# Kernel optimization log

Measured on AMD Instinct MI355X. Metric: run time of the kernel, lower is better.

The kernel has to match this reference:

```python
import jax, jax.numpy as jnp
import numpy as np

B, N, X_DIM, Y_DIM = 256, 128, 8, 8
Z_DIM, R_DIM, HID = 64, 128, 256
STEPS = 50
SIGMA_SQ = 0.5 ** 2
EPSILON = 1.0


def setup_inputs() -> dict:
    key = jax.random.key(0)
    ks = jax.random.split(key, 20)
    s = lambda fan_in: 1.0 / np.sqrt(fan_in)
    inp = {
        'x_ctx': jax.random.normal(ks[0], (B, N, X_DIM), jnp.float32),
        'y_ctx': jax.random.normal(ks[1], (B, N, Y_DIM), jnp.float32),
        'mask': jnp.ones((B, N, 1), jnp.float32),
        'z0': jax.random.normal(ks[2], (B, Z_DIM), jnp.float32),
        'noise': jax.random.normal(ks[3], (STEPS, B, Z_DIM), jnp.float32),
        # encoder: pointwise MLP on [x,y] then masked mean pool, project to r_dim
        'We1': jax.random.normal(ks[4], (X_DIM + Y_DIM, HID), jnp.float32) * s(X_DIM + Y_DIM),
        'be1': jnp.zeros((HID,), jnp.float32),
        'We2': jax.random.normal(ks[5], (HID, R_DIM), jnp.float32) * s(HID),
        'be2': jnp.zeros((R_DIM,), jnp.float32),
        # decoder: MLP([x, z]) -> y per context point
        'Wd1': jax.random.normal(ks[6], (X_DIM + Z_DIM, HID), jnp.float32) * s(X_DIM + Z_DIM),
        'bd1': jnp.zeros((HID,), jnp.float32),
        'Wd2': jax.random.normal(ks[7], (HID, Y_DIM), jnp.float32) * s(HID),
        'bd2': jnp.zeros((Y_DIM,), jnp.float32),
        # drift net: MLP([z, r, t]) -> z_dim
        'Wb1': jax.random.normal(ks[8], (Z_DIM + R_DIM + 1, HID), jnp.float32) * s(Z_DIM + R_DIM + 1),
        'bb1': jnp.zeros((HID,), jnp.float32),
        'Wb2': jax.random.normal(ks[9], (HID, Z_DIM), jnp.float32) * s(HID),
        'bb2': jnp.zeros((Z_DIM,), jnp.float32),
    }
    return inp


def _encode(x, y, mask, We1, be1, We2, be2):
    phi = jax.nn.gelu(jnp.concatenate([x, y], axis=-1) @ We1 + be1)  # [B,N,H]
    pooled = (phi * mask).sum(axis=1) / jnp.maximum(mask.sum(axis=1), 1.0)  # [B,H]
    return pooled @ We2 + be2  # [B,R]


def _decode(z, x, Wd1, bd1, Wd2, bd2):
    zb = jnp.broadcast_to(z[:, None, :], (z.shape[0], x.shape[1], z.shape[1]))
    h = jax.nn.gelu(jnp.concatenate([x, zb], axis=-1) @ Wd1 + bd1)  # [B,N,H]
    return h @ Wd2 + bd2  # [B,N,Y]


def _drift(z, r, t_col, Wb1, bb1, Wb2, bb2):
    h = jax.nn.gelu(jnp.concatenate([z, r, t_col], axis=-1) @ Wb1 + bb1)
    return h @ Wb2 + bb2  # [B,Z]


def reference(x_ctx, y_ctx, mask, z0, noise,
              We1, be1, We2, be2, Wd1, bd1, Wd2, bd2, Wb1, bb1, Wb2, bb2):
    dt = 1.0 / STEPS
    r = _encode(x_ctx, y_ctx, mask, We1, be1, We2, be2)  # [B,R]

    def energy_sum(z, t):
        u0 = 0.5 * jnp.sum(z ** 2, axis=1)  # [B]
        mu_y = _decode(z, x_ctx, Wd1, bd1, Wd2, bd2)
        sse = jnp.sum(((y_ctx - mu_y) ** 2) * mask, axis=(1, 2))  # [B]
        u1 = 0.5 * sse / SIGMA_SQ + u0
        return jnp.sum((1.0 - t) * u0 + t * u1)

    grad_energy = jax.grad(energy_sum, argnums=0)
    t_steps = (jnp.arange(STEPS, dtype=jnp.float32) * dt)
    noise_scale = jnp.sqrt(jnp.float32(2.0 * EPSILON * dt))

    def step(z, xs):
        t_curr, eps_noise = xs
        grad_u = jnp.clip(grad_energy(z, t_curr), -100.0, 100.0)
        t_col = jnp.full((z.shape[0], 1), t_curr, dtype=z.dtype)
        b = _drift(z, r, t_col, Wb1, bb1, Wb2, bb2)
        dz = (-EPSILON * grad_u + b) * dt + noise_scale * eps_noise
        return z + dz, None

    z_final, _ = jax.lax.scan(step, z0, (t_steps, noise))
    return z_final
```

## Files before the change

### kernel.cpp

```cpp
#include <hip/hip_runtime.h>
#include <math.h>

#define BB    256
#define NN_   128
#define ZD    64
#define RD    128
#define HID   256
#define NSTEPS 50
#define NT    16
#define NTILES 8
#define TPB   1024
#define PADD  258

__device__ __forceinline__ double fast_exp_d(double x) {
    const double L2E   = 1.44269504088896340736;
    const double LN2HI = 6.93147180369123816490e-01;
    const double LN2LO = 1.90821492927058770002e-10;
    const double MAGIC = 6755399441055744.0;
    double vn = fma(x, L2E, MAGIC);
    int ni = __double2loint(vn);
    double n = vn - MAGIC;
    double r = fma(n, -LN2HI, x);
    r = fma(n, -LN2LO, r);
    double p = 2.50521083854417187751e-08;
    p = fma(p, r, 2.75573192239858906526e-07);
    p = fma(p, r, 2.75573192239858906526e-06);
    p = fma(p, r, 2.48015873015873015873e-05);
    p = fma(p, r, 1.98412698412698412698e-04);
    p = fma(p, r, 1.38888888888888888889e-03);
    p = fma(p, r, 8.33333333333333333333e-03);
    p = fma(p, r, 4.16666666666666666667e-02);
    p = fma(p, r, 1.66666666666666666667e-01);
    p = fma(p, r, 0.5);
    p = fma(p, r, 1.0);
    p = fma(p, r, 1.0);
    return p * __hiloint2double((1023 + ni) << 20, 0);
}

__device__ __forceinline__ double sigmoid_d(double w) {
    double wc = fmin(fmax(w, -60.0), 60.0);
    double e = fast_exp_d(-wc);
    double d = 1.0 + e;
    float r0 = __builtin_amdgcn_rcpf((float)d);
    double y = (double)r0;
    y = fma(y, fma(-d, y, 1.0), y);
    y = fma(y, fma(-d, y, 1.0), y);
    return y;
}

__device__ __forceinline__ double gelu_d(double x) {
    const double c2 = 1.59576912160573071176;
    double w = c2 * x * fma(0.044715, x * x, 1.0);
    return x * sigmoid_d(w);
}

__device__ __forceinline__ void gelu_both_d(double x, double& h, double& gp) {
    const double c  = 0.79788456080286535588;
    const double a  = 0.044715;
    double x2 = x * x;
    double w  = (2.0 * c) * x * fma(a, x2, 1.0);
    double hp = sigmoid_d(w);
    h = x * hp;
    double s = hp * (1.0 - hp);
    gp = fma(x * s, (2.0 * c) * fma(3.0 * a, x2, 1.0), hp);
}

struct Smem {
    double h_t[NT][PADD];
    float  wd2t_f[8][PADD];
    double z_ds[ZD];
    double hb_ds[HID];
    double scratch4[4][HID];
    double pmgz[1024];
    double res_r[NT][8];
    double bp_d[16][ZD];
    double bd2_d[8];
    double bb2_d[ZD];
    double hbt_s[HID];
    double wbt_s[HID];
    float  bd1_s[HID];
    float  x_s[NN_][8];
    float  y_s[NN_][8];
    float  m_s[NN_];
    __align__(16) float4 wd1z4[HID][16];
};

__global__ void __launch_bounds__(TPB)
nets_sampler_kernel(
    const float* __restrict__ x_ctx, const float* __restrict__ y_ctx,
    const float* __restrict__ mask,  const float* __restrict__ z0,
    const float* __restrict__ noise,
    const float* __restrict__ We1, const float* __restrict__ be1,
    const float* __restrict__ We2, const float* __restrict__ be2,
    const float* __restrict__ Wd1, const float* __restrict__ bd1,
    const float* __restrict__ Wd2, const float* __restrict__ bd2,
    const float* __restrict__ Wb1, const float* __restrict__ bb1,
    const float* __restrict__ Wb2, const float* __restrict__ bb2,
    float* __restrict__ out)
{
    extern __shared__ char smem_raw[];
    Smem& sm = *reinterpret_cast<Smem*>(smem_raw);

    const int b   = blockIdx.x;
    const int tid = threadIdx.x;
    const int j   = tid & 255;
    const int q2  = tid >> 8;
    const int du_k = tid & 63, du_c = tid >> 6;
    double* r_d = &sm.res_r[0][0];

    if (tid < 256) {
        reinterpret_cast<float4*>(&sm.x_s[0][0])[tid] =
            reinterpret_cast<const float4*>(x_ctx + (size_t)b * NN_ * 8)[tid];
        reinterpret_cast<float4*>(&sm.y_s[0][0])[tid] =
            reinterpret_cast<const float4*>(y_ctx + (size_t)b * NN_ * 8)[tid];
        sm.bd1_s[j] = bd1[j];
        float4 a0 = reinterpret_cast<const float4*>(Wd2 + (size_t)j * 8)[0];
        float4 a1 = reinterpret_cast<const float4*>(Wd2 + (size_t)j * 8)[1];
        sm.wd2t_f[0][j] = a0.x; sm.wd2t_f[1][j] = a0.y;
        sm.wd2t_f[2][j] = a0.z; sm.wd2t_f[3][j] = a0.w;
        sm.wd2t_f[4][j] = a1.x; sm.wd2t_f[5][j] = a1.y;
        sm.wd2t_f[6][j] = a1.z; sm.wd2t_f[7][j] = a1.w;
    }
    if (tid < NN_) sm.m_s[tid] = mask[(size_t)b * NN_ + tid];
    if (tid < ZD) {
        sm.z_ds[tid]  = (double)z0[(size_t)b * ZD + tid];
        sm.bb2_d[tid] = (double)bb2[tid];
    }
    if (tid < 8) sm.bd2_d[tid] = (double)bd2[tid];

#pragma unroll
    for (int kk = 0; kk < 16; kk++) {
        const int k = q2 * 16 + kk;
        const float v = Wd1[(8 + k) * HID + j];
        reinterpret_cast<float*>(&sm.wd1z4[j][0])[4 * ((k >> 2) ^ (j & 15)) + (k & 3)] = v;
    }

    float wd1x[8];
#pragma unroll
    for (int k = 0; k < 8; k++) wd1x[k] = Wd1[k * HID + j];

    __syncthreads();

    if (tid < 256) {
        float we1r[16];
#pragma unroll
        for (int k = 0; k < 16; k++) we1r[k] = We1[k * HID + j];
        double be1_d = (double)be1[j];
        double msum = 0.0;
        for (int n = 0; n < NN_; n++) msum += (double)sm.m_s[n];
        msum = fmax(msum, 1.0);
        double pacc = 0.0;
        for (int n = 0; n < NN_; n++) {
            double pre = be1_d;
#pragma unroll
            for (int k = 0; k < 8; k++) pre = fma((double)sm.x_s[n][k], (double)we1r[k], pre);
#pragma unroll
            for (int k = 0; k < 8; k++) pre = fma((double)sm.y_s[n][k], (double)we1r[8 + k], pre);
            pacc += gelu_d(pre) * (double)sm.m_s[n];
        }
        sm.hb_ds[j] = pacc / msum;
    }
    __syncthreads();
    if (tid < 256) {
        int i = tid & 127, half = tid >> 7;
        double racc = 0.0;
        for (int jj = half * 128; jj < half * 128 + 128; jj++)
            racc = fma(sm.hb_ds[jj], (double)We2[jj * RD + i], racc);
        sm.scratch4[half][i] = racc;
    }
    __syncthreads();
    if (tid < RD) r_d[tid] = sm.scratch4[0][tid] + sm.scratch4[1][tid] + (double)be2[tid];
    __syncthreads();

    if (tid < 256) {
        double hbr = (double)bb1[j];
        for (int k = 0; k < RD; k++)
            hbr = fma(r_d[k], (double)Wb1[(ZD + k) * HID + j], hbr);
        sm.hbt_s[j] = hbr;
        sm.wbt_s[j] = (double)Wb1[(ZD + RD) * HID + j];
    }
    __syncthreads();

    const double dt  = 1.0 / (double)NSTEPS;
    const double nsc = sqrt(2.0 * 1.0 * dt);

    for (int s = 0; s < NSTEPS; s++) {
        const double t = (double)s * dt;

        float nzf = 0.0f;
        if (tid < ZD) nzf = noise[((size_t)s * BB + b) * ZD + tid];

        double zd0 = 0.0, zd1 = 0.0;
#pragma unroll 4
        for (int q = 0; q < 16; q++) {
            float4 wv = sm.wd1z4[j][q ^ (j & 15)];
            const int k = q * 4;
            zd0 = fma(sm.z_ds[k],     (double)wv.x, zd0);
            zd1 = fma(sm.z_ds[k + 1], (double)wv.y, zd1);
            zd0 = fma(sm.z_ds[k + 2], (double)wv.z, zd0);
            zd1 = fma(sm.z_ds[k + 3], (double)wv.w, zd1);
        }
        const double zpre = (double)sm.bd1_s[j] + zd0 + zd1;

        {
            double a0 = 0.0;
            const int kb = q2 * 16;
            const float* wb1p = Wb1 + kb * HID + j;
#pragma unroll 8
            for (int kk = 0; kk < 16; kk++)
                a0 = fma(sm.z_ds[kb + kk], (double)wb1p[kk * HID], a0);
            sm.scratch4[q2][j] = a0;
        }
        __syncthreads();
        if (tid < 256) {
            double hacc = sm.hbt_s[j] + t * sm.wbt_s[j]
                        + sm.scratch4[0][j] + sm.scratch4[1][j]
                        + sm.scratch4[2][j] + sm.scratch4[3][j];
            sm.hb_ds[j] = gelu_d(hacc);
        }
        __syncthreads();
        {
            double acc = 0.0;
            const float* wb2p = Wb2 + (du_c * 16) * ZD + du_k;
#pragma unroll 8
            for (int i = 0; i < 16; i++)
                acc = fma(sm.hb_ds[du_c * 16 + i], (double)wb2p[i * ZD], acc);
            sm.bp_d[du_c][du_k] = acc;
        }

        double S = 0.0;
        const int rb = q2 * 4;
        float gp_r0, gp_r1, gp_r2, gp_r3;

        for (int tile = 0; tile < NTILES; tile++) {
            const int xb = tile * NT + rb;
            {
                const float4 xa = *reinterpret_cast<const float4*>(&sm.x_s[xb + 0][0]);
                const float4 xxb = *reinterpret_cast<const float4*>(&sm.x_s[xb + 0][4]);
                const float4 xc = *reinterpret_cast<const float4*>(&sm.x_s[xb + 1][0]);
                const float4 xd = *reinterpret_cast<const float4*>(&sm.x_s[xb + 1][4]);
                double p0 = zpre, p1 = zpre;
                p0 = fma((double)xa.x, (double)wd1x[0], p0);
                p0 = fma((double)xa.y, (double)wd1x[1], p0);
                p0 = fma((double)xa.z, (double)wd1x[2], p0);
                p0 = fma((double)xa.w, (double)wd1x[3], p0);
                p0 = fma((double)xxb.x, (double)wd1x[4], p0);
                p0 = fma((double)xxb.y, (double)wd1x[5], p0);
                p0 = fma((double)xxb.z, (double)wd1x[6], p0);
                p0 = fma((double)xxb.w, (double)wd1x[7], p0);
                p1 = fma((double)xc.x, (double)wd1x[0], p1);
                p1 = fma((double)xc.y, (double)wd1x[1], p1);
                p1 = fma((double)xc.z, (double)wd1x[2], p1);
                p1 = fma((double)xc.w, (double)wd1x[3], p1);
                p1 = fma((double)xd.x, (double)wd1x[4], p1);
                p1 = fma((double)xd.y, (double)wd1x[5], p1);
                p1 = fma((double)xd.z, (double)wd1x[6], p1);
                p1 = fma((double)xd.w, (double)wd1x[7], p1);
                double h0, g0, h1, g1;
                gelu_both_d(p0, h0, g0);
                gelu_both_d(p1, h1, g1);
                sm.h_t[rb + 0][j] = h0; gp_r0 = (float)g0;
                sm.h_t[rb + 1][j] = h1; gp_r1 = (float)g1;
            }
            {
                const float4 xa = *reinterpret_cast<const float4*>(&sm.x_s[xb + 2][0]);
                const float4 xxb = *reinterpret_cast<const float4*>(&sm.x_s[xb + 2][4]);
                const float4 xc = *reinterpret_cast<const float4*>(&sm.x_s[xb + 3][0]);
                const float4 xd = *reinterpret_cast<const float4*>(&sm.x_s[xb + 3][4]);
                double p0 = zpre, p1 = zpre;
                p0 = fma((double)xa.x, (double)wd1x[0], p0);
                p0 = fma((double)xa.y, (double)wd1x[1], p0);
                p0 = fma((double)xa.z, (double)wd1x[2], p0);
                p0 = fma((double)xa.w, (double)wd1x[3], p0);
                p0 = fma((double)xxb.x, (double)wd1x[4], p0);
                p0 = fma((double)xxb.y, (double)wd1x[5], p0);
                p0 = fma((double)xxb.z, (double)wd1x[6], p0);
                p0 = fma((double)xxb.w, (double)wd1x[7], p0);
                p1 = fma((double)xc.x, (double)wd1x[0], p1);
                p1 = fma((double)xc.y, (double)wd1x[1], p1);
                p1 = fma((double)xc.z, (double)wd1x[2], p1);
                p1 = fma((double)xc.w, (double)wd1x[3], p1);
                p1 = fma((double)xd.x, (double)wd1x[4], p1);
                p1 = fma((double)xd.y, (double)wd1x[5], p1);
                p1 = fma((double)xd.z, (double)wd1x[6], p1);
                p1 = fma((double)xd.w, (double)wd1x[7], p1);
                double h0, g0, h1, g1;
                gelu_both_d(p0, h0, g0);
                gelu_both_d(p1, h1, g1);
                sm.h_t[rb + 2][j] = h0; gp_r2 = (float)g0;
                sm.h_t[rb + 3][j] = h1; gp_r3 = (float)g1;
            }
            __syncthreads();
            {
                const int q = tid >> 7, pair = tid & 127;
                const int nn = pair >> 3, yd = pair & 7;
                const double2* hrow = reinterpret_cast<const double2*>(&sm.h_t[nn][q * 32]);
                const float2*  wrow = reinterpret_cast<const float2*>(&sm.wd2t_f[yd][q * 32]);
                double a0 = 0.0, a1 = 0.0;
#pragma unroll 8
                for (int i = 0; i < 16; i++) {
                    double2 hv = hrow[i];
                    float2  wv = wrow[i];
                    a0 = fma(hv.x, (double)wv.x, a0);
                    a1 = fma(hv.y, (double)wv.y, a1);
                }
                sm.pmgz[q * 128 + pair] = a0 + a1;
            }
            __syncthreads();
            if (tid < 128) {
                const int nn = tid >> 3, yd = tid & 7;
                double mu = sm.bd2_d[yd];
#pragma unroll
                for (int q = 0; q < 8; q++) mu += sm.pmgz[q * 128 + tid];
                sm.res_r[nn][yd] = 4.0 * t * (mu - (double)sm.y_s[tile * NT + nn][yd])
                                           * (double)sm.m_s[tile * NT + nn];
            }
            __syncthreads();
            {
                const float w0 = sm.wd2t_f[0][j], w1 = sm.wd2t_f[1][j];
                const float w2 = sm.wd2t_f[2][j], w3 = sm.wd2t_f[3][j];
                const float w4 = sm.wd2t_f[4][j], w5 = sm.wd2t_f[5][j];
                const float w6 = sm.wd2t_f[6][j], w7 = sm.wd2t_f[7][j];
                const double2* rr0 = reinterpret_cast<const double2*>(&sm.res_r[rb + 0][0]);
                const double2* rr1 = reinterpret_cast<const double2*>(&sm.res_r[rb + 1][0]);
                const double2* rr2 = reinterpret_cast<const double2*>(&sm.res_r[rb + 2][0]);
                const double2* rr3 = reinterpret_cast<const double2*>(&sm.res_r[rb + 3][0]);
                double2 a0, a1, a2, a3;
                a0 = rr0[0]; a1 = rr0[1]; a2 = rr0[2]; a3 = rr0[3];
                double dh0 = a0.x * (double)w0 + a0.y * (double)w1
                           + a1.x * (double)w2 + a1.y * (double)w3
                           + a2.x * (double)w4 + a2.y * (double)w5
                           + a3.x * (double)w6 + a3.y * (double)w7;
                S = fma(dh0, (double)gp_r0, S);
                a0 = rr1[0]; a1 = rr1[1]; a2 = rr1[2]; a3 = rr1[3];
                double dh1 = a0.x * (double)w0 + a0.y * (double)w1
                           + a1.x * (double)w2 + a1.y * (double)w3
                           + a2.x * (double)w4 + a2.y * (double)w5
                           + a3.x * (double)w6 + a3.y * (double)w7;
                S = fma(dh1, (double)gp_r1, S);
                a0 = rr2[0]; a1 = rr2[1]; a2 = rr2[2]; a3 = rr2[3];
                double dh2 = a0.x * (double)w0 + a0.y * (double)w1
                           + a1.x * (double)w2 + a1.y * (double)w3
                           + a2.x * (double)w4 + a2.y * (double)w5
                           + a3.x * (double)w6 + a3.y * (double)w7;
                S = fma(dh2, (double)gp_r2, S);
                a0 = rr3[0]; a1 = rr3[1]; a2 = rr3[2]; a3 = rr3[3];
                double dh3 = a0.x * (double)w0 + a0.y * (double)w1
                           + a1.x * (double)w2 + a1.y * (double)w3
                           + a2.x * (double)w4 + a2.y * (double)w5
                           + a3.x * (double)w6 + a3.y * (double)w7;
                S = fma(dh3, (double)gp_r3, S);
            }
        }

        sm.scratch4[q2][j] = S;
        __syncthreads();
        {
            const int k = du_k, c = du_c;
            const int qk = k >> 2, ck = k & 3;
            double acc = 0.0;
#pragma unroll 8
            for (int i = 0; i < 16; i++) {
                const int jj = c * 16 + i;
                const float w = reinterpret_cast<const float*>(&sm.wd1z4[jj][0])
                                    [4 * (qk ^ (jj & 15)) + ck];
                const double sv = sm.scratch4[0][jj] + sm.scratch4[1][jj]
                                + sm.scratch4[2][jj] + sm.scratch4[3][jj];
                acc = fma(sv, (double)w, acc);
            }
            sm.pmgz[c * 64 + k] = acc;
        }
        __syncthreads();
        if (tid < ZD) {
            double gsum = sm.z_ds[tid];
#pragma unroll
            for (int c = 0; c < 16; c++) gsum += sm.pmgz[c * 64 + tid];
            gsum = fmin(fmax(gsum, -100.0), 100.0);
            double bdr = sm.bb2_d[tid];
#pragma unroll
            for (int c = 0; c < 16; c++) bdr += sm.bp_d[c][tid];
            sm.z_ds[tid] = sm.z_ds[tid] + (bdr - gsum) * dt + nsc * (double)nzf;
        }
        __syncthreads();
    }

    if (tid < ZD) out[(size_t)b * ZD + tid] = (float)sm.z_ds[tid];
}

extern "C" void kernel_launch(void* const* d_in, const int* in_sizes, int n_in,
                              void* d_out, int out_size, void* d_ws, size_t ws_size,
                              hipStream_t stream) {
    const float* x_ctx = (const float*)d_in[0];
    const float* y_ctx = (const float*)d_in[1];
    const float* maskp = (const float*)d_in[2];
    const float* z0    = (const float*)d_in[3];
    const float* noise = (const float*)d_in[4];
    const float* We1   = (const float*)d_in[5];
    const float* be1   = (const float*)d_in[6];
    const float* We2   = (const float*)d_in[7];
    const float* be2   = (const float*)d_in[8];
    const float* Wd1   = (const float*)d_in[9];
    const float* bd1   = (const float*)d_in[10];
    const float* Wd2   = (const float*)d_in[11];
    const float* bd2   = (const float*)d_in[12];
    const float* Wb1   = (const float*)d_in[13];
    const float* bb1   = (const float*)d_in[14];
    const float* Wb2   = (const float*)d_in[15];
    const float* bb2   = (const float*)d_in[16];
    float* out = (float*)d_out;

    (void)hipFuncSetAttribute((const void*)nets_sampler_kernel,
                              hipFuncAttributeMaxDynamicSharedMemorySize,
                              (int)sizeof(Smem));

    nets_sampler_kernel<<<BB, TPB, sizeof(Smem), stream>>>(
        x_ctx, y_ctx, maskp, z0, noise,
        We1, be1, We2, be2, Wd1, bd1, Wd2, bd2, Wb1, bb1, Wb2, bb2, out);
}
```

Measured before the change: 1.782 ms.

## Split decoder z-projection across thread groups and reduce mu via warp shuffles

The per-step decoder z-projection is now split so that each of the four thread groups computes a quarter of the 64-wide dot product, with partial sums stored in a new shared buffer and combined later. In the per-tile decoder output stage, the eight-way partial sums are reduced with warp xor-shuffles instead of a shared-memory array, a barrier and a 128-thread serial reduction. This removes one __syncthreads per tile and spreads the z-projection work evenly. In exchange it adds shared-memory traffic for the zdp buffer, and the reads are rotated per lane, which changes the bank access pattern.

```diff
diff --git a/kernel.cpp b/kernel.cpp
--- a/kernel.cpp
+++ b/kernel.cpp
@@ -71,6 +71,7 @@
     double z_ds[ZD];
     double hb_ds[HID];
     double scratch4[4][HID];
+    double zdp[4][HID];
     double pmgz[1024];
     double res_r[NT][8];
     double bp_d[16][ZD];
@@ -184,23 +185,13 @@
     const double dt  = 1.0 / (double)NSTEPS;
     const double nsc = sqrt(2.0 * 1.0 * dt);
 
+    const int mr_nn = tid >> 6, mr_yd = (tid >> 3) & 7, mr_q = tid & 7;
+
     for (int s = 0; s < NSTEPS; s++) {
         const double t = (double)s * dt;
 
         float nzf = 0.0f;
         if (tid < ZD) nzf = noise[((size_t)s * BB + b) * ZD + tid];
-
-        double zd0 = 0.0, zd1 = 0.0;
-#pragma unroll 4
-        for (int q = 0; q < 16; q++) {
-            float4 wv = sm.wd1z4[j][q ^ (j & 15)];
-            const int k = q * 4;
-            zd0 = fma(sm.z_ds[k],     (double)wv.x, zd0);
-            zd1 = fma(sm.z_ds[k + 1], (double)wv.y, zd1);
-            zd0 = fma(sm.z_ds[k + 2], (double)wv.z, zd0);
-            zd1 = fma(sm.z_ds[k + 3], (double)wv.w, zd1);
-        }
-        const double zpre = (double)sm.bd1_s[j] + zd0 + zd1;
 
         {
             double a0 = 0.0;
@@ -210,6 +201,18 @@
             for (int kk = 0; kk < 16; kk++)
                 a0 = fma(sm.z_ds[kb + kk], (double)wb1p[kk * HID], a0);
             sm.scratch4[q2][j] = a0;
+
+            double zq0 = 0.0, zq1 = 0.0;
+#pragma unroll
+            for (int q = q2 * 4; q < q2 * 4 + 4; q++) {
+                float4 wv = sm.wd1z4[j][q ^ (j & 15)];
+                const int k = q * 4;
+                zq0 = fma(sm.z_ds[k],     (double)wv.x, zq0);
+                zq1 = fma(sm.z_ds[k + 1], (double)wv.y, zq1);
+                zq0 = fma(sm.z_ds[k + 2], (double)wv.z, zq0);
+                zq1 = fma(sm.z_ds[k + 3], (double)wv.w, zq1);
+            }
+            sm.zdp[q2][j] = zq0 + zq1;
         }
         __syncthreads();
         if (tid < 256) {
@@ -227,6 +230,9 @@
                 acc = fma(sm.hb_ds[du_c * 16 + i], (double)wb2p[i * ZD], acc);
             sm.bp_d[du_c][du_k] = acc;
         }
+
+        const double zpre = (double)sm.bd1_s[j]
+            + ((sm.zdp[0][j] + sm.zdp[1][j]) + (sm.zdp[2][j] + sm.zdp[3][j]));
 
         double S = 0.0;
         const int rb = q2 * 4;
@@ -292,28 +298,30 @@
             }
             __syncthreads();
             {
-                const int q = tid >> 7, pair = tid & 127;
-                const int nn = pair >> 3, yd = pair & 7;
-                const double2* hrow = reinterpret_cast<const double2*>(&sm.h_t[nn][q * 32]);
-                const float2*  wrow = reinterpret_cast<const float2*>(&sm.wd2t_f[yd][q * 32]);
+                const double2* hrow =
+                    reinterpret_cast<const double2*>(&sm.h_t[mr_nn][mr_q * 32]);
+                const float2*  wrow =
+                    reinterpret_cast<const float2*>(&sm.wd2t_f[mr_yd][mr_q * 32]);
                 double a0 = 0.0, a1 = 0.0;
 #pragma unroll 8
-                for (int i = 0; i < 16; i++) {
-                    double2 hv = hrow[i];
-                    float2  wv = wrow[i];
+                for (int d = 0; d < 16; d++) {
+                    const int dd = (d + 2 * mr_q) & 15;
+                    double2 hv = hrow[dd];
+                    float2  wv = wrow[dd];
                     a0 = fma(hv.x, (double)wv.x, a0);
                     a1 = fma(hv.y, (double)wv.y, a1);
                 }
-                sm.pmgz[q * 128 + pair] = a0 + a1;
-            }
-            __syncthreads();
-            if (tid < 128) {
-                const int nn = tid >> 3, yd = tid & 7;
-                double mu = sm.bd2_d[yd];
-#pragma unroll
-                for (int q = 0; q < 8; q++) mu += sm.pmgz[q * 128 + tid];
-                sm.res_r[nn][yd] = 4.0 * t * (mu - (double)sm.y_s[tile * NT + nn][yd])
-                                           * (double)sm.m_s[tile * NT + nn];
+                double v = a0 + a1;
+                v += __shfl_xor(v, 1);
+                v += __shfl_xor(v, 2);
+                v += __shfl_xor(v, 4);
+                if (mr_q == 0) {
+                    const int row = tile * NT + mr_nn;
+                    double mu = v + sm.bd2_d[mr_yd];
+                    sm.res_r[mr_nn][mr_yd] =
+                        4.0 * t * (mu - (double)sm.y_s[row][mr_yd])
+                                * (double)sm.m_s[row];
+                }
             }
             __syncthreads();
             {
```

After: 1.841 ms. +3.3%, slower.
